# Optimization experiments

Hardware: AMD Instinct MI355X
Metric: run time of the kernel (lower is better)

## Reference

```python
import jax, jax.numpy as jnp
import numpy as np

E = 256   # hidden_dim
H = 2     # num_heads
DH = E // H
EPS = 1e-5


def setup_inputs() -> dict:
    key = jax.random.key(0)
    ks = jax.random.split(key, 20)
    L, S, MAXLOOP = 8192, 8192, 16
    rel = jax.random.randint(ks[0], (L, MAXLOOP), 0, S)
    # sprinkle some padding sentinels (-1 / -2) like real edge loops
    pad = jax.random.uniform(ks[1], (L, MAXLOOP)) < 0.25
    rel = jnp.where(pad, -1, rel)
    rel = rel.at[:, 0].set(jnp.abs(rel[:, 0]) % S)  # ensure >=1 valid edge per face
    inp = {
        'v_face_edge_loop': rel.astype(jnp.int64) if jax.config.jax_enable_x64 else rel.astype(jnp.int32),
        'v_face_mask': jnp.ones((L,), dtype=bool),
        'v_edge_embedding': jax.random.normal(ks[2], (S, E), jnp.float32),
        'v_face_embedding': jax.random.normal(ks[3], (L, E), jnp.float32),
    }
    def w(k, shape):
        return (jax.random.normal(k, shape, jnp.float32) * 0.02)
    for i, base in ((1, 4), (2, 10)):
        inp[f'w_in{i}'] = w(ks[base + 0], (3 * E, E))
        inp[f'b_in{i}'] = jnp.zeros((3 * E,), jnp.float32)
        inp[f'w_out{i}'] = w(ks[base + 1], (E, E))
        inp[f'b_out{i}'] = jnp.zeros((E,), jnp.float32)
        inp[f'ln{i}_g'] = jnp.ones((E,), jnp.float32)
        inp[f'ln{i}_b'] = jnp.zeros((E,), jnp.float32)
    return inp


def _build_mask(face_edge_loop, S):
    # True = disallowed (torch bool attn_mask semantics).
    L = face_edge_loop.shape[0]
    rel = face_edge_loop
    invalid = (rel == -1) | (rel == -2)
    rel = jnp.where(invalid, S, rel)  # scatter invalids into sentinel column S
    mask = jnp.ones((L, S + 1), dtype=bool)
    mask = mask.at[jnp.arange(L)[:, None], rel].set(False)
    return mask[:, :S]  # [L, S]


def _mha(x, kv, mask, w_in, b_in, w_out, b_out):
    # torch nn.MultiheadAttention (unbatched, eval/no-dropout)
    wq, wk, wv = jnp.split(w_in, 3, axis=0)
    bq, bk, bv = jnp.split(b_in, 3, axis=0)
    L, S = x.shape[0], kv.shape[0]
    q = (x @ wq.T + bq).reshape(L, H, DH)
    k = (kv @ wk.T + bk).reshape(S, H, DH)
    v = (kv @ wv.T + bv).reshape(S, H, DH)
    scores = jnp.einsum('lhd,shd->hls', q, k) / np.sqrt(DH).astype(np.float32)
    scores = jnp.where(mask[None, :, :], jnp.float32(-1e9), scores)
    attn = jax.nn.softmax(scores, axis=-1)          # [H, L, S]
    out = jnp.einsum('hls,shd->lhd', attn, v).reshape(L, E)
    return out @ w_out.T + b_out


def _layernorm(x, g, b):
    m = x.mean(-1, keepdims=True)
    var = ((x - m) ** 2).mean(-1, keepdims=True)
    return (x - m) / jnp.sqrt(var + EPS) * g + b


def reference(v_face_edge_loop, v_face_mask, v_edge_embedding, v_face_embedding,
              w_in1, b_in1, w_out1, b_out1, ln1_g, ln1_b,
              w_in2, b_in2, w_out2, b_out2, ln2_g, ln2_b):
    S = v_edge_embedding.shape[0]
    # v_face_mask is all-True here (static shapes); loop[mask] == loop
    mask = _build_mask(v_face_edge_loop, S)
    x = v_face_embedding
    x = x + _mha(x, v_edge_embedding, mask, w_in1, b_in1, w_out1, b_out1)
    x = _layernorm(x, ln1_g, ln1_b)
    x = x + _mha(x, v_edge_embedding, mask, w_in2, b_in2, w_out2, b_out2)
    x = _layernorm(x, ln2_g, ln2_b)
    return x
```

## Files before the change

kernel.cpp:

```cpp
#include <hip/hip_runtime.h>
#include <hip/hip_bf16.h>

typedef short short8 __attribute__((ext_vector_type(8)));
typedef short short4v __attribute__((ext_vector_type(4)));
typedef float f32x4 __attribute__((ext_vector_type(4)));

#define E 256
#define DH 128

__device__ __forceinline__ float bf2f(__hip_bfloat16 x) { return __bfloat162float(x); }
__device__ __forceinline__ __hip_bfloat16 f2bf(float x) { return __float2bfloat16(x); }

struct CvtArgs { const float* in[6]; __hip_bfloat16* out[6]; int n[6]; };

__global__ __launch_bounds__(256) void f2b_all(CvtArgs a)
{
    int seg = blockIdx.y;
    int i = (blockIdx.x * 256 + threadIdx.x) * 8;
    if (i >= a.n[seg]) return;
    const float* in = a.in[seg];
    float4 x = *reinterpret_cast<const float4*>(in + i);
    float4 y = *reinterpret_cast<const float4*>(in + i + 4);
    __hip_bfloat16* o = a.out[seg] + i;
    o[0] = f2bf(x.x); o[1] = f2bf(x.y); o[2] = f2bf(x.z); o[3] = f2bf(x.w);
    o[4] = f2bf(y.x); o[5] = f2bf(y.y); o[6] = f2bf(y.z); o[7] = f2bf(y.w);
}

struct ProjSeg { const __hip_bfloat16* A; const __hip_bfloat16* W; const float* b; __hip_bfloat16* out; };
struct ProjArgs { ProjSeg seg[5]; };

__global__ __launch_bounds__(256) void gemm_proj(ProjArgs args, int M)
{
    int wv = threadIdx.x >> 6, lane = threadIdx.x & 63;
    int m0 = blockIdx.x * 32;
    if (m0 >= M) return;
    ProjSeg sg = args.seg[blockIdx.y];
    int lo = lane & 15, hi = lane >> 4;

    const __hip_bfloat16* arow0 = sg.A + (size_t)(m0 + lo) * E + hi * 8;
    const __hip_bfloat16* arow1 = arow0 + 16 * E;
    const __hip_bfloat16* brow  = sg.W + (size_t)(wv * 64 + lo) * E + hi * 8;

    f32x4 acc[2][4] = {};
#pragma unroll
    for (int k = 0; k < 8; ++k) {
        short8 a0 = *reinterpret_cast<const short8*>(arow0 + k * 32);
        short8 a1 = *reinterpret_cast<const short8*>(arow1 + k * 32);
#pragma unroll
        for (int nt = 0; nt < 4; ++nt) {
            short8 b = *reinterpret_cast<const short8*>(brow + (size_t)nt * 16 * E + k * 32);
            acc[0][nt] = __builtin_amdgcn_mfma_f32_16x16x32_bf16(a0, b, acc[0][nt], 0, 0, 0);
            acc[1][nt] = __builtin_amdgcn_mfma_f32_16x16x32_bf16(a1, b, acc[1][nt], 0, 0, 0);
        }
    }
#pragma unroll
    for (int nt = 0; nt < 4; ++nt) {
        int col = wv * 64 + nt * 16 + lo;
        float bias = sg.b[col];
#pragma unroll
        for (int mt = 0; mt < 2; ++mt)
#pragma unroll
            for (int r = 0; r < 4; ++r) {
                int row = m0 + mt * 16 + hi * 4 + r;
                sg.out[(size_t)row * E + col] = f2bf(acc[mt][nt][r] + bias);
            }
    }
}

__global__ __launch_bounds__(1024) void attn_outproj_ln(
    const int* __restrict__ rel, const __hip_bfloat16* __restrict__ q16,
    const __hip_bfloat16* __restrict__ k16, const __hip_bfloat16* __restrict__ v16,
    const __hip_bfloat16* __restrict__ wout, const float* __restrict__ bout,
    const float* __restrict__ resid, const float* __restrict__ lng, const float* __restrict__ lnb,
    float* __restrict__ xres_out, __hip_bfloat16* __restrict__ xbf_out,
    float* __restrict__ final_out, int L, int ML)
{
    __shared__ __align__(16) __hip_bfloat16 atile[16 * 264];
    __shared__ __align__(16) float sm[16 * 260];
    __shared__ __align__(16) float lds_w[16][2][16];
    __shared__ int lds_idx[16][16];

    int tid = threadIdx.x, wv = tid >> 6, lane = tid & 63;
    int m0 = blockIdx.x * 16;
    int g = lane >> 2, q = lane & 3;
    int face = m0 + wv;
    const float scale = 0.088388347648318447f;

    const int* rr = rel + (size_t)face * ML;
    int myidx = (g < ML) ? rr[g] : -1;

    bool dup = false;
#pragma unroll
    for (int d = 1; d < 16; ++d) {
        int other = __shfl(myidx, ((g - d) & 15) * 4 + q);
        if (d <= g && other == myidx) dup = true;
    }
    bool myuse = (myidx >= 0) && !dup;
    int safe = myidx < 0 ? 0 : myidx;
    if (q == 0) lds_idx[wv][g] = safe;

#pragma unroll
    for (int h = 0; h < 2; ++h) {
        const __hip_bfloat16* kbase = k16 + (size_t)safe * E + h * DH;
        const __hip_bfloat16* qbase = q16 + (size_t)face * E + h * DH;
        float part = 0.f;
#pragma unroll
        for (int t = 0; t < 4; ++t) {
            short8 qv = *reinterpret_cast<const short8*>(qbase + (t * 4 + q) * 8);
            short8 kv = *reinterpret_cast<const short8*>(kbase + (t * 4 + q) * 8);
            const __hip_bfloat16* qp = (const __hip_bfloat16*)&qv;
            const __hip_bfloat16* kp = (const __hip_bfloat16*)&kv;
#pragma unroll
            for (int e2 = 0; e2 < 8; ++e2)
                part += bf2f(qp[e2]) * bf2f(kp[e2]);
        }
        part += __shfl_xor(part, 1);
        part += __shfl_xor(part, 2);
        float sc = myuse ? part * scale : -1e30f;
        float mx = sc;
#pragma unroll
        for (int off = 4; off < 64; off <<= 1) mx = fmaxf(mx, __shfl_xor(mx, off));
        float e = __expf(sc - mx);
        float den = e;
#pragma unroll
        for (int off = 4; off < 64; off <<= 1) den += __shfl_xor(den, off);
        if (q == 0) lds_w[wv][h][g] = e / den;
    }

    {
        int h = lane >> 5;
        float a0 = 0.f, a1 = 0.f, a2 = 0.f, a3 = 0.f;
#pragma unroll
        for (int j = 0; j < 16; ++j) {
            int ij = lds_idx[wv][j];
            float wj = lds_w[wv][h][j];
            short4v vv = *reinterpret_cast<const short4v*>(v16 + (size_t)ij * E + 4 * lane);
            const __hip_bfloat16* vp = (const __hip_bfloat16*)&vv;
            a0 += wj * bf2f(vp[0]);
            a1 += wj * bf2f(vp[1]);
            a2 += wj * bf2f(vp[2]);
            a3 += wj * bf2f(vp[3]);
        }
        __hip_bfloat16 ob[4] = {f2bf(a0), f2bf(a1), f2bf(a2), f2bf(a3)};
        *reinterpret_cast<short4v*>(atile + wv * 264 + 4 * lane) =
            *reinterpret_cast<const short4v*>(ob);
    }
    __syncthreads();

    {
        int lo = lane & 15, hi = lane >> 4;
        const __hip_bfloat16* arow = atile + lo * 264 + hi * 8;
        const __hip_bfloat16* brow = wout + (size_t)(wv * 16 + lo) * E + hi * 8;
        f32x4 acc = {0.f, 0.f, 0.f, 0.f};
#pragma unroll
        for (int kk = 0; kk < 8; ++kk) {
            short8 a = *reinterpret_cast<const short8*>(arow + kk * 32);
            short8 b = *reinterpret_cast<const short8*>(brow + kk * 32);
            acc = __builtin_amdgcn_mfma_f32_16x16x32_bf16(a, b, acc, 0, 0, 0);
        }
        int col = wv * 16 + lo;
#pragma unroll
        for (int r = 0; r < 4; ++r)
            sm[(hi * 4 + r) * 260 + col] = acc[r];
    }
    __syncthreads();

    {
        int rowg = m0 + wv;
        float4 pv = *reinterpret_cast<const float4*>(sm + wv * 260 + 4 * lane);
        float4 rv = *reinterpret_cast<const float4*>(resid + (size_t)rowg * E + 4 * lane);
        float4 bb = *reinterpret_cast<const float4*>(bout + 4 * lane);
        float v0 = pv.x + bb.x + rv.x;
        float v1 = pv.y + bb.y + rv.y;
        float v2 = pv.z + bb.z + rv.z;
        float v3 = pv.w + bb.w + rv.w;
        float s  = v0 + v1 + v2 + v3;
        float s2 = v0 * v0 + v1 * v1 + v2 * v2 + v3 * v3;
#pragma unroll
        for (int off = 1; off < 64; off <<= 1) {
            s  += __shfl_xor(s, off);
            s2 += __shfl_xor(s2, off);
        }
        float mean = s * (1.f / 256.f);
        float var  = s2 * (1.f / 256.f) - mean * mean;
        float rstd = rsqrtf(var + 1e-5f);
        float4 gg = *reinterpret_cast<const float4*>(lng + 4 * lane);
        float4 b2 = *reinterpret_cast<const float4*>(lnb + 4 * lane);
        float y0 = (v0 - mean) * rstd * gg.x + b2.x;
        float y1 = (v1 - mean) * rstd * gg.y + b2.y;
        float y2 = (v2 - mean) * rstd * gg.z + b2.z;
        float y3 = (v3 - mean) * rstd * gg.w + b2.w;
        if (final_out) {
            float4 o = {y0, y1, y2, y3};
            *reinterpret_cast<float4*>(final_out + (size_t)rowg * E + 4 * lane) = o;
        } else {
            float4 o = {y0, y1, y2, y3};
            *reinterpret_cast<float4*>(xres_out + (size_t)rowg * E + 4 * lane) = o;
            __hip_bfloat16 ob[4] = {f2bf(y0), f2bf(y1), f2bf(y2), f2bf(y3)};
            *reinterpret_cast<short4v*>(xbf_out + (size_t)rowg * E + 4 * lane) =
                *reinterpret_cast<const short4v*>(ob);
        }
    }
}

extern "C" void kernel_launch(void* const* d_in, const int* in_sizes, int n_in,
                              void* d_out, int out_size, void* d_ws, size_t ws_size,
                              hipStream_t stream) {
    const int* rel = (const int*)d_in[0];
    const float* edge = (const float*)d_in[2];
    const float* face = (const float*)d_in[3];
    const float* w_in[2]  = {(const float*)d_in[4],  (const float*)d_in[10]};
    const float* b_in[2]  = {(const float*)d_in[5],  (const float*)d_in[11]};
    const float* w_out[2] = {(const float*)d_in[6],  (const float*)d_in[12]};
    const float* b_out[2] = {(const float*)d_in[7],  (const float*)d_in[13]};
    const float* ln_g[2]  = {(const float*)d_in[8],  (const float*)d_in[14]};
    const float* ln_b[2]  = {(const float*)d_in[9],  (const float*)d_in[15]};

    int S = in_sizes[2] / E;
    int L = in_sizes[3] / E;
    int ML = in_sizes[0] / L;

    char* ws = (char*)d_ws;
    __hip_bfloat16* face16 = (__hip_bfloat16*)ws; ws += (size_t)L * E * 2;
    __hip_bfloat16* edge16 = (__hip_bfloat16*)ws; ws += (size_t)S * E * 2;
    __hip_bfloat16* q16    = (__hip_bfloat16*)ws; ws += (size_t)L * E * 2;
    __hip_bfloat16* k16[2], *v16[2];
    for (int l = 0; l < 2; ++l) {
        k16[l] = (__hip_bfloat16*)ws; ws += (size_t)S * E * 2;
        v16[l] = (__hip_bfloat16*)ws; ws += (size_t)S * E * 2;
    }
    __hip_bfloat16* xbf = (__hip_bfloat16*)ws;    ws += (size_t)L * E * 2;
    float* xres = (float*)ws;                     ws += (size_t)L * E * 4;
    __hip_bfloat16* win16[2], *wout16[2];
    for (int l = 0; l < 2; ++l) {
        win16[l]  = (__hip_bfloat16*)ws; ws += (size_t)3 * E * E * 2;
        wout16[l] = (__hip_bfloat16*)ws; ws += (size_t)E * E * 2;
    }

    float* outp = (float*)d_out;

    {
        CvtArgs ca;
        ca.in[0] = face;     ca.out[0] = face16;    ca.n[0] = L * E;
        ca.in[1] = edge;     ca.out[1] = edge16;    ca.n[1] = S * E;
        ca.in[2] = w_in[0];  ca.out[2] = win16[0];  ca.n[2] = 3 * E * E;
        ca.in[3] = w_in[1];  ca.out[3] = win16[1];  ca.n[3] = 3 * E * E;
        ca.in[4] = w_out[0]; ca.out[4] = wout16[0]; ca.n[4] = E * E;
        ca.in[5] = w_out[1]; ca.out[5] = wout16[1]; ca.n[5] = E * E;
        int gx = (L * E) / (256 * 8);
        f2b_all<<<dim3(gx, 6), 256, 0, stream>>>(ca);
    }

    {
        ProjArgs pa;
        pa.seg[0] = {face16, win16[0],                     b_in[0],         q16};
        pa.seg[1] = {edge16, win16[0] + (size_t)E * E,     b_in[0] + E,     k16[0]};
        pa.seg[2] = {edge16, win16[0] + (size_t)2 * E * E, b_in[0] + 2 * E, v16[0]};
        pa.seg[3] = {edge16, win16[1] + (size_t)E * E,     b_in[1] + E,     k16[1]};
        pa.seg[4] = {edge16, win16[1] + (size_t)2 * E * E, b_in[1] + 2 * E, v16[1]};
        gemm_proj<<<dim3(L / 32, 5), 256, 0, stream>>>(pa, L);
    }

    attn_outproj_ln<<<L / 16, 1024, 0, stream>>>(rel, q16, k16[0], v16[0],
                                                 wout16[0], b_out[0], face,
                                                 ln_g[0], ln_b[0],
                                                 xres, xbf, nullptr, L, ML);

    {
        ProjArgs pa;
        pa.seg[0] = {xbf, win16[1], b_in[1], q16};
        gemm_proj<<<dim3(L / 32, 1), 256, 0, stream>>>(pa, L);
    }

    attn_outproj_ln<<<L / 16, 1024, 0, stream>>>(rel, q16, k16[1], v16[1],
                                                 wout16[1], b_out[1], xres,
                                                 ln_g[1], ln_b[1],
                                                 nullptr, nullptr, outp, L, ML);
}
```

Baseline: 182.8 us.

## Fuse Q projections and both attention layers into one per-tile kernel

Both Q projections (from face embeddings and from the layer-1 output) move into a single fused kernel that keeps the face tile and intermediate activations in LDS. This cuts the launch sequence from five kernels to three and removes the global round-trips for q16, xres and xbf, along with the face fp32-to-bf16 conversion pass. The conversion kernel now also writes bf16 with vector stores. In exchange, each block does a small 16-row MFMA for Q, which uses the W_q weights less efficiently than the 32-row GEMM did, and the kernel's LDS use and register pressure go up.

```diff
diff --git a/kernel.cpp b/kernel.cpp
--- a/kernel.cpp
+++ b/kernel.cpp
@@ -11,7 +11,13 @@
 __device__ __forceinline__ float bf2f(__hip_bfloat16 x) { return __bfloat162float(x); }
 __device__ __forceinline__ __hip_bfloat16 f2bf(float x) { return __float2bfloat16(x); }
 
-struct CvtArgs { const float* in[6]; __hip_bfloat16* out[6]; int n[6]; };
+__device__ __forceinline__ short8 cvt8(float4 a, float4 b) {
+    __hip_bfloat16 t[8] = {f2bf(a.x), f2bf(a.y), f2bf(a.z), f2bf(a.w),
+                           f2bf(b.x), f2bf(b.y), f2bf(b.z), f2bf(b.w)};
+    return *reinterpret_cast<const short8*>(t);
+}
+
+struct CvtArgs { const float* in[5]; __hip_bfloat16* out[5]; int n[5]; };
 
 __global__ __launch_bounds__(256) void f2b_all(CvtArgs a)
 {
@@ -21,13 +27,11 @@
     const float* in = a.in[seg];
     float4 x = *reinterpret_cast<const float4*>(in + i);
     float4 y = *reinterpret_cast<const float4*>(in + i + 4);
-    __hip_bfloat16* o = a.out[seg] + i;
-    o[0] = f2bf(x.x); o[1] = f2bf(x.y); o[2] = f2bf(x.z); o[3] = f2bf(x.w);
-    o[4] = f2bf(y.x); o[5] = f2bf(y.y); o[6] = f2bf(y.z); o[7] = f2bf(y.w);
-}
-
-struct ProjSeg { const __hip_bfloat16* A; const __hip_bfloat16* W; const float* b; __hip_bfloat16* out; };
-struct ProjArgs { ProjSeg seg[5]; };
+    *reinterpret_cast<short8*>(a.out[seg] + i) = cvt8(x, y);
+}
+
+struct ProjSeg { const __hip_bfloat16* W; const float* b; __hip_bfloat16* out; };
+struct ProjArgs { const __hip_bfloat16* A; ProjSeg seg[4]; };
 
 __global__ __launch_bounds__(256) void gemm_proj(ProjArgs args, int M)
 {
@@ -37,15 +41,15 @@
     ProjSeg sg = args.seg[blockIdx.y];
     int lo = lane & 15, hi = lane >> 4;
 
-    const __hip_bfloat16* arow0 = sg.A + (size_t)(m0 + lo) * E + hi * 8;
-    const __hip_bfloat16* arow1 = arow0 + 16 * E;
-    const __hip_bfloat16* brow  = sg.W + (size_t)(wv * 64 + lo) * E + hi * 8;
+    const __hip_bfloat16* ar0 = args.A + (size_t)(m0 + lo) * E + hi * 8;
+    const __hip_bfloat16* ar1 = ar0 + 16 * E;
+    const __hip_bfloat16* brow = sg.W + (size_t)(wv * 64 + lo) * E + hi * 8;
 
     f32x4 acc[2][4] = {};
 #pragma unroll
     for (int k = 0; k < 8; ++k) {
-        short8 a0 = *reinterpret_cast<const short8*>(arow0 + k * 32);
-        short8 a1 = *reinterpret_cast<const short8*>(arow1 + k * 32);
+        short8 a0 = *reinterpret_cast<const short8*>(ar0 + k * 32);
+        short8 a1 = *reinterpret_cast<const short8*>(ar1 + k * 32);
 #pragma unroll
         for (int nt = 0; nt < 4; ++nt) {
             short8 b = *reinterpret_cast<const short8*>(brow + (size_t)nt * 16 * E + k * 32);
@@ -67,14 +71,20 @@
     }
 }
 
-__global__ __launch_bounds__(1024) void attn_outproj_ln(
-    const int* __restrict__ rel, const __hip_bfloat16* __restrict__ q16,
-    const __hip_bfloat16* __restrict__ k16, const __hip_bfloat16* __restrict__ v16,
-    const __hip_bfloat16* __restrict__ wout, const float* __restrict__ bout,
-    const float* __restrict__ resid, const float* __restrict__ lng, const float* __restrict__ lnb,
-    float* __restrict__ xres_out, __hip_bfloat16* __restrict__ xbf_out,
-    float* __restrict__ final_out, int L, int ML)
+__global__ __launch_bounds__(1024) void mega_fused(
+    const int* __restrict__ rel, const float* __restrict__ facef,
+    const __hip_bfloat16* __restrict__ wq0, const float* __restrict__ bq0,
+    const __hip_bfloat16* __restrict__ k0, const __hip_bfloat16* __restrict__ v0,
+    const __hip_bfloat16* __restrict__ wout0, const float* __restrict__ bout0,
+    const float* __restrict__ ln0g, const float* __restrict__ ln0b,
+    const __hip_bfloat16* __restrict__ wq1, const float* __restrict__ bq1,
+    const __hip_bfloat16* __restrict__ k1, const __hip_bfloat16* __restrict__ v1,
+    const __hip_bfloat16* __restrict__ wout1, const float* __restrict__ bout1,
+    const float* __restrict__ ln1g, const float* __restrict__ ln1b,
+    float* __restrict__ outp, int L, int ML)
 {
+    __shared__ __align__(16) __hip_bfloat16 ftile[16 * 264];
+    __shared__ __align__(16) __hip_bfloat16 qtile[16 * 264];
     __shared__ __align__(16) __hip_bfloat16 atile[16 * 264];
     __shared__ __align__(16) float sm[16 * 260];
     __shared__ __align__(16) float lds_w[16][2][16];
@@ -84,11 +94,11 @@
     int m0 = blockIdx.x * 16;
     int g = lane >> 2, q = lane & 3;
     int face = m0 + wv;
+    int lo = lane & 15, hi = lane >> 4;
     const float scale = 0.088388347648318447f;
 
     const int* rr = rel + (size_t)face * ML;
     int myidx = (g < ML) ? rr[g] : -1;
-
     bool dup = false;
 #pragma unroll
     for (int d = 1; d < 16; ++d) {
@@ -99,107 +109,150 @@
     int safe = myidx < 0 ? 0 : myidx;
     if (q == 0) lds_idx[wv][g] = safe;
 
-#pragma unroll
-    for (int h = 0; h < 2; ++h) {
-        const __hip_bfloat16* kbase = k16 + (size_t)safe * E + h * DH;
-        const __hip_bfloat16* qbase = q16 + (size_t)face * E + h * DH;
-        float part = 0.f;
-#pragma unroll
-        for (int t = 0; t < 4; ++t) {
-            short8 qv = *reinterpret_cast<const short8*>(qbase + (t * 4 + q) * 8);
-            short8 kv = *reinterpret_cast<const short8*>(kbase + (t * 4 + q) * 8);
-            const __hip_bfloat16* qp = (const __hip_bfloat16*)&qv;
-            const __hip_bfloat16* kp = (const __hip_bfloat16*)&kv;
-#pragma unroll
-            for (int e2 = 0; e2 < 8; ++e2)
-                part += bf2f(qp[e2]) * bf2f(kp[e2]);
-        }
-        part += __shfl_xor(part, 1);
-        part += __shfl_xor(part, 2);
-        float sc = myuse ? part * scale : -1e30f;
-        float mx = sc;
-#pragma unroll
-        for (int off = 4; off < 64; off <<= 1) mx = fmaxf(mx, __shfl_xor(mx, off));
-        float e = __expf(sc - mx);
-        float den = e;
-#pragma unroll
-        for (int off = 4; off < 64; off <<= 1) den += __shfl_xor(den, off);
-        if (q == 0) lds_w[wv][h][g] = e / den;
-    }
-
     {
-        int h = lane >> 5;
-        float a0 = 0.f, a1 = 0.f, a2 = 0.f, a3 = 0.f;
-#pragma unroll
-        for (int j = 0; j < 16; ++j) {
-            int ij = lds_idx[wv][j];
-            float wj = lds_w[wv][h][j];
-            short4v vv = *reinterpret_cast<const short4v*>(v16 + (size_t)ij * E + 4 * lane);
-            const __hip_bfloat16* vp = (const __hip_bfloat16*)&vv;
-            a0 += wj * bf2f(vp[0]);
-            a1 += wj * bf2f(vp[1]);
-            a2 += wj * bf2f(vp[2]);
-            a3 += wj * bf2f(vp[3]);
-        }
-        __hip_bfloat16 ob[4] = {f2bf(a0), f2bf(a1), f2bf(a2), f2bf(a3)};
-        *reinterpret_cast<short4v*>(atile + wv * 264 + 4 * lane) =
-            *reinterpret_cast<const short4v*>(ob);
+        float4 fv = *reinterpret_cast<const float4*>(facef + (size_t)face * E + 4 * lane);
+        __hip_bfloat16 fb[4] = {f2bf(fv.x), f2bf(fv.y), f2bf(fv.z), f2bf(fv.w)};
+        *reinterpret_cast<short4v*>(ftile + wv * 264 + 4 * lane) =
+            *reinterpret_cast<const short4v*>(fb);
     }
     __syncthreads();
 
-    {
-        int lo = lane & 15, hi = lane >> 4;
-        const __hip_bfloat16* arow = atile + lo * 264 + hi * 8;
-        const __hip_bfloat16* brow = wout + (size_t)(wv * 16 + lo) * E + hi * 8;
-        f32x4 acc = {0.f, 0.f, 0.f, 0.f};
-#pragma unroll
-        for (int kk = 0; kk < 8; ++kk) {
-            short8 a = *reinterpret_cast<const short8*>(arow + kk * 32);
-            short8 b = *reinterpret_cast<const short8*>(brow + kk * 32);
-            acc = __builtin_amdgcn_mfma_f32_16x16x32_bf16(a, b, acc, 0, 0, 0);
-        }
-        int col = wv * 16 + lo;
-#pragma unroll
-        for (int r = 0; r < 4; ++r)
-            sm[(hi * 4 + r) * 260 + col] = acc[r];
-    }
-    __syncthreads();
-
-    {
-        int rowg = m0 + wv;
-        float4 pv = *reinterpret_cast<const float4*>(sm + wv * 260 + 4 * lane);
-        float4 rv = *reinterpret_cast<const float4*>(resid + (size_t)rowg * E + 4 * lane);
-        float4 bb = *reinterpret_cast<const float4*>(bout + 4 * lane);
-        float v0 = pv.x + bb.x + rv.x;
-        float v1 = pv.y + bb.y + rv.y;
-        float v2 = pv.z + bb.z + rv.z;
-        float v3 = pv.w + bb.w + rv.w;
-        float s  = v0 + v1 + v2 + v3;
-        float s2 = v0 * v0 + v1 * v1 + v2 * v2 + v3 * v3;
-#pragma unroll
-        for (int off = 1; off < 64; off <<= 1) {
-            s  += __shfl_xor(s, off);
-            s2 += __shfl_xor(s2, off);
-        }
-        float mean = s * (1.f / 256.f);
-        float var  = s2 * (1.f / 256.f) - mean * mean;
-        float rstd = rsqrtf(var + 1e-5f);
-        float4 gg = *reinterpret_cast<const float4*>(lng + 4 * lane);
-        float4 b2 = *reinterpret_cast<const float4*>(lnb + 4 * lane);
-        float y0 = (v0 - mean) * rstd * gg.x + b2.x;
-        float y1 = (v1 - mean) * rstd * gg.y + b2.y;
-        float y2 = (v2 - mean) * rstd * gg.z + b2.z;
-        float y3 = (v3 - mean) * rstd * gg.w + b2.w;
-        if (final_out) {
-            float4 o = {y0, y1, y2, y3};
-            *reinterpret_cast<float4*>(final_out + (size_t)rowg * E + 4 * lane) = o;
-        } else {
-            float4 o = {y0, y1, y2, y3};
-            *reinterpret_cast<float4*>(xres_out + (size_t)rowg * E + 4 * lane) = o;
-            __hip_bfloat16 ob[4] = {f2bf(y0), f2bf(y1), f2bf(y2), f2bf(y3)};
-            *reinterpret_cast<short4v*>(xbf_out + (size_t)rowg * E + 4 * lane) =
+    float yk[4];
+
+#pragma unroll
+    for (int layer = 0; layer < 2; ++layer) {
+        const __hip_bfloat16* wq    = layer ? wq1 : wq0;
+        const float*          bq    = layer ? bq1 : bq0;
+        const __hip_bfloat16* kk16  = layer ? k1 : k0;
+        const __hip_bfloat16* vv16  = layer ? v1 : v0;
+        const __hip_bfloat16* wo    = layer ? wout1 : wout0;
+        const float*          bo    = layer ? bout1 : bout0;
+        const float*          lg    = layer ? ln1g : ln0g;
+        const float*          lb    = layer ? ln1b : ln0b;
+
+        {
+            const __hip_bfloat16* arow = ftile + lo * 264 + hi * 8;
+            const __hip_bfloat16* brow = wq + (size_t)(wv * 16 + lo) * E + hi * 8;
+            f32x4 acc = {0.f, 0.f, 0.f, 0.f};
+#pragma unroll
+            for (int kki = 0; kki < 8; ++kki) {
+                short8 a = *reinterpret_cast<const short8*>(arow + kki * 32);
+                short8 b = *reinterpret_cast<const short8*>(brow + kki * 32);
+                acc = __builtin_amdgcn_mfma_f32_16x16x32_bf16(a, b, acc, 0, 0, 0);
+            }
+            int col = wv * 16 + lo;
+            float bias = bq[col];
+#pragma unroll
+            for (int r = 0; r < 4; ++r)
+                qtile[(hi * 4 + r) * 264 + col] = f2bf(acc[r] + bias);
+        }
+        __syncthreads();
+
+#pragma unroll
+        for (int h = 0; h < 2; ++h) {
+            const __hip_bfloat16* kbase = kk16 + (size_t)safe * E + h * DH;
+            const __hip_bfloat16* qbase = qtile + wv * 264 + h * DH;
+            float part = 0.f;
+#pragma unroll
+            for (int t = 0; t < 4; ++t) {
+                short8 qv = *reinterpret_cast<const short8*>(qbase + (t * 4 + q) * 8);
+                short8 kv = *reinterpret_cast<const short8*>(kbase + (t * 4 + q) * 8);
+                const __hip_bfloat16* qp = (const __hip_bfloat16*)&qv;
+                const __hip_bfloat16* kp = (const __hip_bfloat16*)&kv;
+#pragma unroll
+                for (int e2 = 0; e2 < 8; ++e2)
+                    part += bf2f(qp[e2]) * bf2f(kp[e2]);
+            }
+            part += __shfl_xor(part, 1);
+            part += __shfl_xor(part, 2);
+            float sc = myuse ? part * scale : -1e30f;
+            float mx = sc;
+#pragma unroll
+            for (int off = 4; off < 64; off <<= 1) mx = fmaxf(mx, __shfl_xor(mx, off));
+            float e = __expf(sc - mx);
+            float den = e;
+#pragma unroll
+            for (int off = 4; off < 64; off <<= 1) den += __shfl_xor(den, off);
+            if (q == 0) lds_w[wv][h][g] = e / den;
+        }
+        {
+            int h = lane >> 5;
+            float a0 = 0.f, a1 = 0.f, a2 = 0.f, a3 = 0.f;
+#pragma unroll
+            for (int j = 0; j < 16; ++j) {
+                int ij = lds_idx[wv][j];
+                float wj = lds_w[wv][h][j];
+                short4v vv = *reinterpret_cast<const short4v*>(vv16 + (size_t)ij * E + 4 * lane);
+                const __hip_bfloat16* vp = (const __hip_bfloat16*)&vv;
+                a0 += wj * bf2f(vp[0]);
+                a1 += wj * bf2f(vp[1]);
+                a2 += wj * bf2f(vp[2]);
+                a3 += wj * bf2f(vp[3]);
+            }
+            __hip_bfloat16 ob[4] = {f2bf(a0), f2bf(a1), f2bf(a2), f2bf(a3)};
+            *reinterpret_cast<short4v*>(atile + wv * 264 + 4 * lane) =
                 *reinterpret_cast<const short4v*>(ob);
         }
+        __syncthreads();
+
+        {
+            const __hip_bfloat16* arow = atile + lo * 264 + hi * 8;
+            const __hip_bfloat16* brow = wo + (size_t)(wv * 16 + lo) * E + hi * 8;
+            f32x4 acc = {0.f, 0.f, 0.f, 0.f};
+#pragma unroll
+            for (int kki = 0; kki < 8; ++kki) {
+                short8 a = *reinterpret_cast<const short8*>(arow + kki * 32);
+                short8 b = *reinterpret_cast<const short8*>(brow + kki * 32);
+                acc = __builtin_amdgcn_mfma_f32_16x16x32_bf16(a, b, acc, 0, 0, 0);
+            }
+            int col = wv * 16 + lo;
+#pragma unroll
+            for (int r = 0; r < 4; ++r)
+                sm[(hi * 4 + r) * 260 + col] = acc[r];
+        }
+        __syncthreads();
+
+        {
+            float4 pv = *reinterpret_cast<const float4*>(sm + wv * 260 + 4 * lane);
+            float4 bb = *reinterpret_cast<const float4*>(bo + 4 * lane);
+            float r0, r1, r2, r3;
+            if (layer == 0) {
+                float4 rv = *reinterpret_cast<const float4*>(facef + (size_t)face * E + 4 * lane);
+                r0 = rv.x; r1 = rv.y; r2 = rv.z; r3 = rv.w;
+            } else {
+                r0 = yk[0]; r1 = yk[1]; r2 = yk[2]; r3 = yk[3];
+            }
+            float v0 = pv.x + bb.x + r0;
+            float v1 = pv.y + bb.y + r1;
+            float v2 = pv.z + bb.z + r2;
+            float v3 = pv.w + bb.w + r3;
+            float s  = v0 + v1 + v2 + v3;
+            float s2 = v0 * v0 + v1 * v1 + v2 * v2 + v3 * v3;
+#pragma unroll
+            for (int off = 1; off < 64; off <<= 1) {
+                s  += __shfl_xor(s, off);
+                s2 += __shfl_xor(s2, off);
+            }
+            float mean = s * (1.f / 256.f);
+            float var  = s2 * (1.f / 256.f) - mean * mean;
+            float rstd = rsqrtf(var + 1e-5f);
+            float4 gg = *reinterpret_cast<const float4*>(lg + 4 * lane);
+            float4 b2 = *reinterpret_cast<const float4*>(lb + 4 * lane);
+            float y0 = (v0 - mean) * rstd * gg.x + b2.x;
+            float y1 = (v1 - mean) * rstd * gg.y + b2.y;
+            float y2 = (v2 - mean) * rstd * gg.z + b2.z;
+            float y3 = (v3 - mean) * rstd * gg.w + b2.w;
+            if (layer == 0) {
+                yk[0] = y0; yk[1] = y1; yk[2] = y2; yk[3] = y3;
+                __hip_bfloat16 yb[4] = {f2bf(y0), f2bf(y1), f2bf(y2), f2bf(y3)};
+                *reinterpret_cast<short4v*>(ftile + wv * 264 + 4 * lane) =
+                    *reinterpret_cast<const short4v*>(yb);
+            } else {
+                float4 o = {y0, y1, y2, y3};
+                *reinterpret_cast<float4*>(outp + (size_t)face * E + 4 * lane) = o;
+            }
+        }
+        if (layer == 0) __syncthreads();
     }
 }
 
@@ -221,16 +274,12 @@
     int ML = in_sizes[0] / L;
 
     char* ws = (char*)d_ws;
-    __hip_bfloat16* face16 = (__hip_bfloat16*)ws; ws += (size_t)L * E * 2;
     __hip_bfloat16* edge16 = (__hip_bfloat16*)ws; ws += (size_t)S * E * 2;
-    __hip_bfloat16* q16    = (__hip_bfloat16*)ws; ws += (size_t)L * E * 2;
     __hip_bfloat16* k16[2], *v16[2];
     for (int l = 0; l < 2; ++l) {
         k16[l] = (__hip_bfloat16*)ws; ws += (size_t)S * E * 2;
         v16[l] = (__hip_bfloat16*)ws; ws += (size_t)S * E * 2;
     }
-    __hip_bfloat16* xbf = (__hip_bfloat16*)ws;    ws += (size_t)L * E * 2;
-    float* xres = (float*)ws;                     ws += (size_t)L * E * 4;
     __hip_bfloat16* win16[2], *wout16[2];
     for (int l = 0; l < 2; ++l) {
         win16[l]  = (__hip_bfloat16*)ws; ws += (size_t)3 * E * E * 2;
@@ -241,39 +290,29 @@
 
     {
         CvtArgs ca;
-        ca.in[0] = face;     ca.out[0] = face16;    ca.n[0] = L * E;
-        ca.in[1] = edge;     ca.out[1] = edge16;    ca.n[1] = S * E;
-        ca.in[2] = w_in[0];  ca.out[2] = win16[0];  ca.n[2] = 3 * E * E;
-        ca.in[3] = w_in[1];  ca.out[3] = win16[1];  ca.n[3] = 3 * E * E;
-        ca.in[4] = w_out[0]; ca.out[4] = wout16[0]; ca.n[4] = E * E;
-        ca.in[5] = w_out[1]; ca.out[5] = wout16[1]; ca.n[5] = E * E;
-        int gx = (L * E) / (256 * 8);
-        f2b_all<<<dim3(gx, 6), 256, 0, stream>>>(ca);
+        ca.in[0] = edge;     ca.out[0] = edge16;    ca.n[0] = S * E;
+        ca.in[1] = w_in[0];  ca.out[1] = win16[0];  ca.n[1] = 3 * E * E;
+        ca.in[2] = w_in[1];  ca.out[2] = win16[1];  ca.n[2] = 3 * E * E;
+        ca.in[3] = w_out[0]; ca.out[3] = wout16[0]; ca.n[3] = E * E;
+        ca.in[4] = w_out[1]; ca.out[4] = wout16[1]; ca.n[4] = E * E;
+        int gx = (S * E) / (256 * 8);
+        f2b_all<<<dim3(gx, 5), 256, 0, stream>>>(ca);
     }
 
     {
         ProjArgs pa;
-        pa.seg[0] = {face16, win16[0],                     b_in[0],         q16};
-        pa.seg[1] = {edge16, win16[0] + (size_t)E * E,     b_in[0] + E,     k16[0]};
-        pa.seg[2] = {edge16, win16[0] + (size_t)2 * E * E, b_in[0] + 2 * E, v16[0]};
-        pa.seg[3] = {edge16, win16[1] + (size_t)E * E,     b_in[1] + E,     k16[1]};
-        pa.seg[4] = {edge16, win16[1] + (size_t)2 * E * E, b_in[1] + 2 * E, v16[1]};
-        gemm_proj<<<dim3(L / 32, 5), 256, 0, stream>>>(pa, L);
-    }
-
-    attn_outproj_ln<<<L / 16, 1024, 0, stream>>>(rel, q16, k16[0], v16[0],
-                                                 wout16[0], b_out[0], face,
-                                                 ln_g[0], ln_b[0],
-                                                 xres, xbf, nullptr, L, ML);
-
-    {
-        ProjArgs pa;
-        pa.seg[0] = {xbf, win16[1], b_in[1], q16};
-        gemm_proj<<<dim3(L / 32, 1), 256, 0, stream>>>(pa, L);
-    }
-
-    attn_outproj_ln<<<L / 16, 1024, 0, stream>>>(rel, q16, k16[1], v16[1],
-                                                 wout16[1], b_out[1], xres,
-                                                 ln_g[1], ln_b[1],
-                                                 nullptr, nullptr, outp, L, ML);
-}
+        pa.A = edge16;
+        pa.seg[0] = {win16[0] + (size_t)E * E,     b_in[0] + E,     k16[0]};
+        pa.seg[1] = {win16[0] + (size_t)2 * E * E, b_in[0] + 2 * E, v16[0]};
+        pa.seg[2] = {win16[1] + (size_t)E * E,     b_in[1] + E,     k16[1]};
+        pa.seg[3] = {win16[1] + (size_t)2 * E * E, b_in[1] + 2 * E, v16[1]};
+        gemm_proj<<<dim3(S / 32, 4), 256, 0, stream>>>(pa, S);
+    }
+
+    mega_fused<<<L / 16, 1024, 0, stream>>>(rel, face,
+                                            win16[0], b_in[0], k16[0], v16[0],
+                                            wout16[0], b_out[0], ln_g[0], ln_b[0],
+                                            win16[1], b_in[1], k16[1], v16[1],
+                                            wout16[1], b_out[1], ln_g[1], ln_b[1],
+                                            outp, L, ML);
+}
```

Result: no change. 185.2 us (+1.3%).
